# Optimization experiments

Measured on AMD Instinct MI355X. Metric: run time of the kernel, lower is better.

Reference implementation:

```python
import jax, jax.numpy as jnp
import numpy as np

TOPK = 13
ALPHA = 1.0
BETA = 6.0
CENTER_RADIUS = 0.5
EPS = 1e-7
IMG = 2048
STRIDES = (8, 16, 32)


def _make_anchor_points():
    pts = []
    for s in STRIDES:
        n = IMG // s
        c = (jnp.arange(n, dtype=jnp.float32) + 0.5) * s
        yy, xx = jnp.meshgrid(c, c, indexing='ij')
        pts.append(jnp.stack([xx.ravel(), yy.ravel()], axis=-1))
    return jnp.concatenate(pts, axis=0)  # [86016, 2]


def setup_inputs() -> dict:
    key = jax.random.key(0)
    k = jax.random.split(key, 6)
    anchor_points = _make_anchor_points()           # [P, 2]
    P = anchor_points.shape[0]
    C, G = 365, 100
    pred_scores = jax.random.normal(k[0], (P, C), dtype=jnp.float32) * 2.0 - 2.0
    pred_objectness = jax.random.normal(k[1], (P,), dtype=jnp.float32)
    # predicted boxes: anchor +- positive ltrb distances (valid xyxy)
    dist = jax.random.uniform(k[2], (P, 4), minval=2.0, maxval=120.0, dtype=jnp.float32)
    pred_boxes = jnp.concatenate([anchor_points - dist[:, :2], anchor_points + dist[:, 2:]], axis=-1)
    ctr = jax.random.uniform(k[3], (G, 2), minval=64.0, maxval=IMG - 64.0, dtype=jnp.float32)
    half = jax.random.uniform(k[4], (G, 2), minval=16.0, maxval=160.0, dtype=jnp.float32)
    gt_boxes = jnp.concatenate([ctr - half, ctr + half], axis=-1)  # [G, 4] xyxy
    gt_labels = jax.random.randint(k[5], (G,), 0, C, dtype=jnp.int64)
    valid_class_mask = jnp.ones((C,), dtype=bool)
    return {
        'pred_scores': pred_scores,
        'pred_boxes': pred_boxes,
        'pred_objectness': pred_objectness,
        'anchor_points': anchor_points,
        'gt_boxes': gt_boxes,
        'gt_labels': gt_labels,
        'valid_class_mask': valid_class_mask,
    }


def _iou_matrix(gt_boxes, pred_boxes):
    # gt: [G,4], pred: [P,4] -> [G,P]
    lt = jnp.maximum(gt_boxes[:, None, :2], pred_boxes[None, :, :2])
    rb = jnp.minimum(gt_boxes[:, None, 2:], pred_boxes[None, :, 2:])
    wh = jnp.clip(rb - lt, 0.0)
    inter = wh[..., 0] * wh[..., 1]
    area_g = jnp.prod(jnp.clip(gt_boxes[:, 2:] - gt_boxes[:, :2], 0.0), axis=-1)
    area_p = jnp.prod(jnp.clip(pred_boxes[:, 2:] - pred_boxes[:, :2], 0.0), axis=-1)
    union = area_g[:, None] + area_p[None, :] - inter
    return inter / (union + EPS)


def reference(pred_scores, pred_boxes, pred_objectness, anchor_points, gt_boxes, gt_labels, valid_class_mask):
    P, C = pred_scores.shape
    G = gt_boxes.shape[0]
    gt_labels = gt_labels.astype(jnp.int32)

    valid_gt = (gt_labels >= 0) & (gt_labels < C) & valid_class_mask[jnp.clip(gt_labels, 0, C - 1)]

    # inside-box mask [G, P]
    ax, ay = anchor_points[:, 0], anchor_points[:, 1]
    inside = ((ax[None, :] >= gt_boxes[:, 0:1]) & (ax[None, :] <= gt_boxes[:, 2:3]) &
              (ay[None, :] >= gt_boxes[:, 1:2]) & (ay[None, :] <= gt_boxes[:, 3:4]))

    gt_center = (gt_boxes[:, :2] + gt_boxes[:, 2:]) * 0.5               # [G,2]
    half_size = jnp.clip((gt_boxes[:, 2:] - gt_boxes[:, :2]) * 0.5, 1.0)
    center_delta = jnp.abs(anchor_points[None, :, :] - gt_center[:, None, :]) / half_size[:, None, :]  # [G,P,2]
    cd_max = center_delta.max(axis=-1)                                   # [G,P]
    center_mask = cd_max <= CENTER_RADIUS

    strict = inside & center_mask
    has_center = strict.any(axis=1, keepdims=True)                       # [G,1]
    cand = jnp.where(has_center, strict, inside)                         # fallback to inside-only

    iou = _iou_matrix(gt_boxes, pred_boxes)                              # [G,P]
    cls_scores = jax.nn.sigmoid(pred_scores[:, jnp.clip(gt_labels, 0, C - 1)].T)  # [G,P]
    pred_obj = jax.nn.sigmoid(pred_objectness)                           # [P]
    quality = jnp.sqrt(jnp.clip(pred_obj[None, :] * cls_scores, 0.0))
    center_prior = jnp.exp(-0.5 * jnp.sum(center_delta ** 2, axis=-1))   # [G,P]
    align = (quality ** ALPHA) * (iou ** BETA) * center_prior            # [G,P], >= 0

    masked = jnp.where(cand & valid_gt[:, None], align, -1.0)
    top_val, top_idx = jax.lax.top_k(masked, TOPK)                       # [G,TOPK]
    # scatter per-GT top-k back to [G,P]; entries with value -1 (non-candidates) stay excluded
    sel = jnp.full((G, P), -1.0, dtype=align.dtype)
    sel = sel.at[jnp.arange(G)[:, None], top_idx].set(jnp.where(top_val > -0.5, top_val, -1.0))

    # sequential 'override only if strictly greater' == per-point argmax with ties to earliest GT
    metric = sel.max(axis=0)                                             # [P]
    best_gt = jnp.argmax(sel, axis=0)                                    # [P]
    fg_mask = metric > -0.5

    overlap = iou[best_gt, jnp.arange(P)]                                # [P]
    matched_gt_indices = jnp.where(fg_mask, best_gt, -1)
    matched_labels = jnp.where(fg_mask, gt_labels[best_gt], -1)

    target_boxes = jnp.where(fg_mask[:, None], gt_boxes[best_gt], 0.0)   # [P,4]
    lab_idx = jnp.clip(matched_labels, 0, C - 1)
    score_val = jnp.where(fg_mask, jnp.clip(overlap, 0.1), 0.0)
    target_scores = jnp.zeros((P, C), dtype=pred_scores.dtype).at[jnp.arange(P), lab_idx].set(score_val)

    return (target_scores, target_boxes, fg_mask, matched_gt_indices, matched_labels)
```

## Files before the change

### kernel.cpp

```cpp
#include <hip/hip_runtime.h>
#include <cstdint>
#include <cstddef>

#define TOPK 13
#define MAXC 2816
#define NLEV 3
#define NZB  1948

__global__ __launch_bounds__(256) void pdl_zero_topk_kernel(
    const float*  __restrict__ scores,
    const float4* __restrict__ pboxes,
    const float*  __restrict__ obj,
    const float4* __restrict__ gtb,
    const int*    __restrict__ glab,
    const unsigned char* __restrict__ vmask,
    unsigned long long* __restrict__ ws_keys,
    float* __restrict__ out,
    int C, int G, long long nfloat4)
{
    const int bid = blockIdx.x;
    const int tid = threadIdx.x;

    if (bid >= G) {
        float4* dst = (float4*)out;
        const float4 z = make_float4(0.0f, 0.0f, 0.0f, 0.0f);
        const long long chunk = (nfloat4 + NZB - 1) / NZB;
        long long s0 = (long long)(bid - G) * chunk;
        long long s1 = s0 + chunk; if (s1 > nfloat4) s1 = nfloat4;
        for (long long i = s0 + tid; i < s1; i += 1024) {
            dst[i] = z;
            if (i + 256 < s1) dst[i + 256] = z;
            if (i + 512 < s1) dst[i + 512] = z;
            if (i + 768 < s1) dst[i + 768] = z;
        }
        return;
    }

    const int g = bid;
    if (tid < TOPK) ws_keys[g * TOPK + tid] = 0ULL;

    const float4 gb = gtb[g];
    const int lab = glab[g];
    bool valid = (lab >= 0) && (lab < C);
    if (valid) {
        valid = (vmask[lab] != 0) || (vmask[4 * (size_t)lab] != 0) ||
                (vmask[8 * (size_t)lab] != 0);
    }
    if (!valid) return;

    __shared__ int s_flag;
    __shared__ int s_count;
    __shared__ unsigned long long s_merge[4 * TOPK];
    __shared__ unsigned long long s_keys[MAXC];

    if (tid == 0) { s_flag = 0; s_count = 0; }

    const float cx = (gb.x + gb.z) * 0.5f;
    const float cy = (gb.y + gb.w) * 0.5f;
    const float hx = fmaxf((gb.z - gb.x) * 0.5f, 1.0f);
    const float hy = fmaxf((gb.w - gb.y) * 0.5f, 1.0f);
    const float area_g = fmaxf(gb.z - gb.x, 0.0f) * fmaxf(gb.w - gb.y, 0.0f);

    const int ls[NLEV]   = {8, 16, 32};
    const int ln[NLEV]   = {256, 128, 64};
    const int loff[NLEV] = {0, 65536, 81920};
    int x0[NLEV], y0[NLEV], ww[NLEV], cnt[NLEV];
    int T = 0;
    #pragma unroll
    for (int l = 0; l < NLEV; ++l) {
        const float fs = (float)ls[l];
        int xa = (int)floorf(gb.x / fs - 0.5f);
        int xb = (int)ceilf (gb.z / fs - 0.5f);
        int ya = (int)floorf(gb.y / fs - 0.5f);
        int yb = (int)ceilf (gb.w / fs - 0.5f);
        xa = xa > 0 ? xa : 0;
        ya = ya > 0 ? ya : 0;
        xb = xb < ln[l] - 1 ? xb : ln[l] - 1;
        yb = yb < ln[l] - 1 ? yb : ln[l] - 1;
        int w = xb - xa + 1; if (w < 0) w = 0;
        int h = yb - ya + 1; if (h < 0) h = 0;
        x0[l] = xa; y0[l] = ya; ww[l] = w;
        cnt[l] = w * h;
        T += cnt[l];
    }
    __syncthreads();

    bool any_strict = false;
    for (int j = tid; j < T; j += 256) {
        int jj = j, l = 0;
        if (jj >= cnt[0]) { jj -= cnt[0]; l = 1; if (jj >= cnt[1]) { jj -= cnt[1]; l = 2; } }
        const int iy = jj / ww[l];
        const int ix = jj - iy * ww[l];
        const float fs = (float)ls[l];
        const float ax = ((float)(x0[l] + ix) + 0.5f) * fs;
        const float ay = ((float)(y0[l] + iy) + 0.5f) * fs;
        if (ax >= gb.x && ax <= gb.z && ay >= gb.y && ay <= gb.w) {
            const float cdx = fabsf(ax - cx) / hx;
            const float cdy = fabsf(ay - cy) / hy;
            if (fmaxf(cdx, cdy) <= 0.5f) any_strict = true;
        }
    }
    if (any_strict) s_flag = 1;
    __syncthreads();
    const bool has_center = (s_flag != 0);

    for (int j = tid; j < T; j += 256) {
        int jj = j, l = 0;
        if (jj >= cnt[0]) { jj -= cnt[0]; l = 1; if (jj >= cnt[1]) { jj -= cnt[1]; l = 2; } }
        const int iy = jj / ww[l];
        const int ix = jj - iy * ww[l];
        const float fs = (float)ls[l];
        const float ax = ((float)(x0[l] + ix) + 0.5f) * fs;
        const float ay = ((float)(y0[l] + iy) + 0.5f) * fs;
        if (!(ax >= gb.x && ax <= gb.z && ay >= gb.y && ay <= gb.w)) continue;
        const float cdx = fabsf(ax - cx) / hx;
        const float cdy = fabsf(ay - cy) / hy;
        const bool strict = fmaxf(cdx, cdy) <= 0.5f;
        if (has_center && !strict) continue;

        const int p = loff[l] + (y0[l] + iy) * ln[l] + (x0[l] + ix);
        const float4 pb = pboxes[p];
        const float so = 1.0f / (1.0f + expf(-obj[p]));
        const float sc = 1.0f / (1.0f + expf(-scores[(size_t)p * C + lab]));
        const float prior = expf(-0.5f * (cdx * cdx + cdy * cdy));
        const float ltx = fmaxf(gb.x, pb.x);
        const float lty = fmaxf(gb.y, pb.y);
        const float rbx = fminf(gb.z, pb.z);
        const float rby = fminf(gb.w, pb.w);
        const float wi = fmaxf(rbx - ltx, 0.0f);
        const float hi = fmaxf(rby - lty, 0.0f);
        const float inter = wi * hi;
        const float area_p = fmaxf(pb.z - pb.x, 0.0f) * fmaxf(pb.w - pb.y, 0.0f);
        const float iou = inter / (area_g + area_p - inter + 1e-7f);
        const float q = sqrtf(fmaxf(so * sc, 0.0f));
        const float i2 = iou * iou;
        const float align = q * (i2 * i2 * i2) * prior;

        const unsigned long long key =
            ((unsigned long long)__float_as_uint(align) << 32)
          | (unsigned long long)(0xFFFFFFFFu ^ (unsigned)p);
        const int slot = atomicAdd(&s_count, 1);
        if (slot < MAXC) s_keys[slot] = key;
    }
    __syncthreads();
    const int M = s_count < MAXC ? s_count : MAXC;

    const int wid  = tid >> 6;
    const int lane = tid & 63;

    unsigned long long best = 0ULL; int bi = -1;
    for (int i = tid; i < M; i += 256) {
        const unsigned long long k = s_keys[i];
        if (k > best) { best = k; bi = i; }
    }
    for (int r = 0; r < TOPK; ++r) {
        unsigned long long wb = best;
        #pragma unroll
        for (int d = 32; d >= 1; d >>= 1) {
            const unsigned long long o = __shfl_xor(wb, d, 64);
            if (o > wb) wb = o;
        }
        if (lane == 0) s_merge[wid * TOPK + r] = wb;
        if (wb != 0ULL && best == wb) {
            s_keys[bi] = 0ULL;
            best = 0ULL; bi = -1;
            for (int i = tid; i < M; i += 256) {
                const unsigned long long k = s_keys[i];
                if (k > best) { best = k; bi = i; }
            }
        }
    }
    __syncthreads();

    if (wid == 0) {
        unsigned long long v = (lane < 4 * TOPK) ? s_merge[lane] : 0ULL;
        for (int r = 0; r < TOPK; ++r) {
            unsigned long long wb = v;
            #pragma unroll
            for (int d = 32; d >= 1; d >>= 1) {
                const unsigned long long o = __shfl_xor(wb, d, 64);
                if (o > wb) wb = o;
            }
            if (lane == 0) ws_keys[g * TOPK + r] = wb;
            if (v == wb) v = 0ULL;
        }
    }
}

__global__ __launch_bounds__(256) void pdl_finalize_kernel(
    const float4* __restrict__ pboxes,
    const float4* __restrict__ gtb,
    const int*    __restrict__ glab,
    const unsigned long long* __restrict__ ws_keys,
    float* __restrict__ out,
    int P, int C, int G)
{
    const int tid = threadIdx.x;
    const int p0  = blockIdx.x * 256;
    const int p   = p0 + tid;

    __shared__ unsigned long long s_best[256];
    s_best[tid] = 0ULL;
    __syncthreads();

    const int npairs = G * TOPK;
    for (int j = tid; j < npairs; j += 256) {
        const unsigned long long k = ws_keys[j];
        if (k == 0ULL) continue;
        const unsigned pp = 0xFFFFFFFFu ^ (unsigned)(k & 0xFFFFFFFFull);
        const int d = (int)pp - p0;
        if (d >= 0 && d < 256) {
            const int g = j / TOPK;
            const unsigned long long key2 =
                (k & 0xFFFFFFFF00000000ull) |
                (unsigned long long)(0xFFFFFFFFu - (unsigned)g);
            atomicMax(&s_best[d], key2);
        }
    }
    __syncthreads();

    if (p < P) {
        const unsigned long long k = s_best[tid];
        const bool fg = (k != 0ULL);
        float4 tb = make_float4(0.0f, 0.0f, 0.0f, 0.0f);
        float mgi = -1.0f, mlab = -1.0f;
        if (fg) {
            const int bg = (int)(0xFFFFFFFFu - (unsigned)(k & 0xFFFFFFFFull));
            const float4 gbx = gtb[bg];
            const float4 pb  = pboxes[p];
            const float ltx = fmaxf(gbx.x, pb.x);
            const float lty = fmaxf(gbx.y, pb.y);
            const float rbx = fminf(gbx.z, pb.z);
            const float rby = fminf(gbx.w, pb.w);
            const float wi = fmaxf(rbx - ltx, 0.0f);
            const float hi = fmaxf(rby - lty, 0.0f);
            const float inter = wi * hi;
            const float ag = fmaxf(gbx.z - gbx.x, 0.0f) * fmaxf(gbx.w - gbx.y, 0.0f);
            const float ap = fmaxf(pb.z - pb.x, 0.0f) * fmaxf(pb.w - pb.y, 0.0f);
            const float iou = inter / (ag + ap - inter + 1e-7f);
            const int lb = glab[bg];
            tb   = gbx;
            mgi  = (float)bg;
            mlab = (float)lb;
            int lbc = lb < 0 ? 0 : (lb > C - 1 ? C - 1 : lb);
            out[(size_t)p * C + lbc] = fmaxf(iou, 0.1f);
        }
        float4* boxes_out = (float4*)(out + (size_t)P * C);
        boxes_out[p] = tb;
        const size_t base = (size_t)P * C + (size_t)4 * P;
        out[base + p]                 = fg ? 1.0f : 0.0f;
        out[base + (size_t)P + p]     = mgi;
        out[base + (size_t)2 * P + p] = mlab;
    }
}

extern "C" void kernel_launch(void* const* d_in, const int* in_sizes, int n_in,
                              void* d_out, int out_size, void* d_ws, size_t ws_size,
                              hipStream_t stream)
{
    (void)n_in; (void)out_size; (void)ws_size;

    const float*  scores = (const float*)d_in[0];
    const float4* pboxes = (const float4*)d_in[1];
    const float*  obj    = (const float*)d_in[2];
    const float4* gtb    = (const float4*)d_in[4];
    const int*    glab   = (const int*)d_in[5];
    const unsigned char* vmask = (const unsigned char*)d_in[6];

    const int P = in_sizes[2];
    const int C = in_sizes[0] / P;
    const int G = in_sizes[5];

    unsigned long long* ws_keys = (unsigned long long*)d_ws;
    float* out = (float*)d_out;

    const long long nfloat4 = ((long long)P * C) / 4;

    pdl_zero_topk_kernel<<<G + NZB, 256, 0, stream>>>(scores, pboxes, obj, gtb,
                                                      glab, vmask, ws_keys, out,
                                                      C, G, nfloat4);
    pdl_finalize_kernel<<<(P + 255) / 256, 256, 0, stream>>>(pboxes, gtb, glab,
                                                             ws_keys, out, P, C, G);
}
```

Measured before the change: 38.98 us.

## Move score-tensor zeroing into finalize kernel, fusing zero-fill with one-hot writes

The large target_scores zero-fill moves out of the top-k kernel and into the second kernel. Each score block zeroes its own contiguous slice and then writes the one-hot IoU values for the rows it covers, after resolving per-point winners in shared memory. Separate blocks handle the per-point box, mask and index outputs in chunks of 1344 points. The top-k kernel now launches only G blocks. Before, the zero-fill ran concurrently with top-k. Now it is serialized after top-k, and every score block scans all G*TOPK keys, so the overlap is lost in exchange for fusing the scatter writes with the zero-fill.

```diff
diff --git a/kernel.cpp b/kernel.cpp
--- a/kernel.cpp
+++ b/kernel.cpp
@@ -5,9 +5,11 @@
 #define TOPK 13
 #define MAXC 2816
 #define NLEV 3
-#define NZB  1948
-
-__global__ __launch_bounds__(256) void pdl_zero_topk_kernel(
+#define SCB  2016
+#define APB  1344
+#define NROWMAX 64
+
+__global__ __launch_bounds__(256) void pdl_topk_kernel(
     const float*  __restrict__ scores,
     const float4* __restrict__ pboxes,
     const float*  __restrict__ obj,
@@ -15,28 +17,11 @@
     const int*    __restrict__ glab,
     const unsigned char* __restrict__ vmask,
     unsigned long long* __restrict__ ws_keys,
-    float* __restrict__ out,
-    int C, int G, long long nfloat4)
+    int C)
 {
-    const int bid = blockIdx.x;
+    const int g   = blockIdx.x;
     const int tid = threadIdx.x;
 
-    if (bid >= G) {
-        float4* dst = (float4*)out;
-        const float4 z = make_float4(0.0f, 0.0f, 0.0f, 0.0f);
-        const long long chunk = (nfloat4 + NZB - 1) / NZB;
-        long long s0 = (long long)(bid - G) * chunk;
-        long long s1 = s0 + chunk; if (s1 > nfloat4) s1 = nfloat4;
-        for (long long i = s0 + tid; i < s1; i += 1024) {
-            dst[i] = z;
-            if (i + 256 < s1) dst[i + 256] = z;
-            if (i + 512 < s1) dst[i + 512] = z;
-            if (i + 768 < s1) dst[i + 768] = z;
-        }
-        return;
-    }
-
-    const int g = bid;
     if (tid < TOPK) ws_keys[g * TOPK + tid] = 0ULL;
 
     const float4 gb = gtb[g];
@@ -187,7 +172,7 @@
     }
 }
 
-__global__ __launch_bounds__(256) void pdl_finalize_kernel(
+__global__ __launch_bounds__(256) void pdl_write_kernel(
     const float4* __restrict__ pboxes,
     const float4* __restrict__ gtb,
     const int*    __restrict__ glab,
@@ -195,37 +180,50 @@
     float* __restrict__ out,
     int P, int C, int G)
 {
+    const int bid = blockIdx.x;
     const int tid = threadIdx.x;
-    const int p0  = blockIdx.x * 256;
-    const int p   = p0 + tid;
-
-    __shared__ unsigned long long s_best[256];
-    s_best[tid] = 0ULL;
-    __syncthreads();
-
     const int npairs = G * TOPK;
-    for (int j = tid; j < npairs; j += 256) {
-        const unsigned long long k = ws_keys[j];
-        if (k == 0ULL) continue;
-        const unsigned pp = 0xFFFFFFFFu ^ (unsigned)(k & 0xFFFFFFFFull);
-        const int d = (int)pp - p0;
-        if (d >= 0 && d < 256) {
-            const int g = j / TOPK;
-            const unsigned long long key2 =
-                (k & 0xFFFFFFFF00000000ull) |
-                (unsigned long long)(0xFFFFFFFFu - (unsigned)g);
-            atomicMax(&s_best[d], key2);
-        }
-    }
-    __syncthreads();
-
-    if (p < P) {
-        const unsigned long long k = s_best[tid];
-        const bool fg = (k != 0ULL);
-        float4 tb = make_float4(0.0f, 0.0f, 0.0f, 0.0f);
-        float mgi = -1.0f, mlab = -1.0f;
-        if (fg) {
+
+    __shared__ unsigned long long s_best[APB];
+
+    if (bid < SCB) {
+        const long long nf4 = ((long long)P * C) >> 2;
+        const long long chunk = (nf4 + SCB - 1) / SCB;
+        const long long s0 = (long long)bid * chunk;
+        long long s1 = s0 + chunk; if (s1 > nf4) s1 = nf4;
+        if (s0 >= s1) return;
+
+        const int r0 = (int)((s0 * 4) / C);
+        const int r1 = (int)((s1 * 4 - 1) / C);
+        const int nrows = r1 - r0 + 1;
+
+        __shared__ int   s_hcol[NROWMAX];
+        __shared__ float s_hval[NROWMAX];
+        unsigned long long* s_row = s_best;
+
+        for (int i = tid; i < nrows; i += 256) s_row[i] = 0ULL;
+        __syncthreads();
+
+        for (int j = tid; j < npairs; j += 256) {
+            const unsigned long long k = ws_keys[j];
+            if (k == 0ULL) continue;
+            const unsigned pp = 0xFFFFFFFFu ^ (unsigned)(k & 0xFFFFFFFFull);
+            const int d = (int)pp - r0;
+            if (d >= 0 && d < nrows) {
+                const int g = j / TOPK;
+                const unsigned long long key2 =
+                    (k & 0xFFFFFFFF00000000ull) |
+                    (unsigned long long)(0xFFFFFFFFu - (unsigned)g);
+                atomicMax(&s_row[d], key2);
+            }
+        }
+        __syncthreads();
+
+        for (int i = tid; i < nrows; i += 256) {
+            const unsigned long long k = s_row[i];
+            if (k == 0ULL) continue;
             const int bg = (int)(0xFFFFFFFFu - (unsigned)(k & 0xFFFFFFFFull));
+            const int p  = r0 + i;
             const float4 gbx = gtb[bg];
             const float4 pb  = pboxes[p];
             const float ltx = fmaxf(gbx.x, pb.x);
@@ -238,16 +236,70 @@
             const float ag = fmaxf(gbx.z - gbx.x, 0.0f) * fmaxf(gbx.w - gbx.y, 0.0f);
             const float ap = fmaxf(pb.z - pb.x, 0.0f) * fmaxf(pb.w - pb.y, 0.0f);
             const float iou = inter / (ag + ap - inter + 1e-7f);
-            const int lb = glab[bg];
-            tb   = gbx;
+            int lb = glab[bg];
+            lb = lb < 0 ? 0 : (lb > C - 1 ? C - 1 : lb);
+            s_hcol[i] = lb;
+            s_hval[i] = fmaxf(iou, 0.1f);
+        }
+
+        float4* dst = (float4*)out;
+        const float4 z = make_float4(0.0f, 0.0f, 0.0f, 0.0f);
+        for (long long i = s0 + tid; i < s1; i += 1024) {
+            dst[i] = z;
+            if (i + 256 < s1) dst[i + 256] = z;
+            if (i + 512 < s1) dst[i + 512] = z;
+            if (i + 768 < s1) dst[i + 768] = z;
+        }
+        __syncthreads();
+
+        for (int i = tid; i < nrows; i += 256) {
+            if (s_row[i] != 0ULL) {
+                const long long f = (long long)(r0 + i) * C + s_hcol[i];
+                if (f >= s0 * 4 && f < s1 * 4)
+                    out[f] = s_hval[i];
+            }
+        }
+        return;
+    }
+
+    const int a0 = (bid - SCB) * APB;
+    int a1 = a0 + APB; if (a1 > P) a1 = P;
+    const int na = a1 - a0;
+    if (na <= 0) return;
+
+    for (int i = tid; i < na; i += 256) s_best[i] = 0ULL;
+    __syncthreads();
+
+    for (int j = tid; j < npairs; j += 256) {
+        const unsigned long long k = ws_keys[j];
+        if (k == 0ULL) continue;
+        const unsigned pp = 0xFFFFFFFFu ^ (unsigned)(k & 0xFFFFFFFFull);
+        const int d = (int)pp - a0;
+        if (d >= 0 && d < na) {
+            const int g = j / TOPK;
+            const unsigned long long key2 =
+                (k & 0xFFFFFFFF00000000ull) |
+                (unsigned long long)(0xFFFFFFFFu - (unsigned)g);
+            atomicMax(&s_best[d], key2);
+        }
+    }
+    __syncthreads();
+
+    float4* boxes_out = (float4*)(out + (size_t)P * C);
+    const size_t base = (size_t)P * C + (size_t)4 * P;
+    for (int i = tid; i < na; i += 256) {
+        const int p = a0 + i;
+        const unsigned long long k = s_best[i];
+        const bool fg = (k != 0ULL);
+        float4 tb = make_float4(0.0f, 0.0f, 0.0f, 0.0f);
+        float mgi = -1.0f, mlab = -1.0f;
+        if (fg) {
+            const int bg = (int)(0xFFFFFFFFu - (unsigned)(k & 0xFFFFFFFFull));
+            tb   = gtb[bg];
             mgi  = (float)bg;
-            mlab = (float)lb;
-            int lbc = lb < 0 ? 0 : (lb > C - 1 ? C - 1 : lb);
-            out[(size_t)p * C + lbc] = fmaxf(iou, 0.1f);
-        }
-        float4* boxes_out = (float4*)(out + (size_t)P * C);
+            mlab = (float)glab[bg];
+        }
         boxes_out[p] = tb;
-        const size_t base = (size_t)P * C + (size_t)4 * P;
         out[base + p]                 = fg ? 1.0f : 0.0f;
         out[base + (size_t)P + p]     = mgi;
         out[base + (size_t)2 * P + p] = mlab;
@@ -274,11 +326,10 @@
     unsigned long long* ws_keys = (unsigned long long*)d_ws;
     float* out = (float*)d_out;
 
-    const long long nfloat4 = ((long long)P * C) / 4;
-
-    pdl_zero_topk_kernel<<<G + NZB, 256, 0, stream>>>(scores, pboxes, obj, gtb,
-                                                      glab, vmask, ws_keys, out,
-                                                      C, G, nfloat4);
-    pdl_finalize_kernel<<<(P + 255) / 256, 256, 0, stream>>>(pboxes, gtb, glab,
-                                                             ws_keys, out, P, C, G);
+    const int ACB = (P + APB - 1) / APB;
+
+    pdl_topk_kernel<<<G, 256, 0, stream>>>(scores, pboxes, obj, gtb, glab,
+                                           vmask, ws_keys, C);
+    pdl_write_kernel<<<SCB + ACB, 256, 0, stream>>>(pboxes, gtb, glab, ws_keys,
+                                                    out, P, C, G);
 }
```

After: 45.64 us. 1.17x slower.

## Fuse center-check and candidate scoring into one pass with wave-aggregated atomics

Applied to the files above, without the earlier changes.

Merges the two passes over in-box anchors into one: each candidate is scored immediately and tagged with a strict-center bit in the top bit of its sort key, so strict candidates rank above non-strict ones. The strict-only filtering is applied at the end when writing the top-k results. Shared-memory slot allocation now uses one atomic per wavefront via ballot and popcount instead of one per thread. The cost is that non-strict candidates are always scored, and more keys may fill the MAXC buffer.

```diff
diff --git a/kernel.cpp b/kernel.cpp
--- a/kernel.cpp
+++ b/kernel.cpp
@@ -6,6 +6,7 @@
 #define MAXC 2816
 #define NLEV 3
 #define NZB  1948
+#define STRICT_BIT 0x8000000000000000ull
 
 __global__ __launch_bounds__(256) void pdl_zero_topk_kernel(
     const float*  __restrict__ scores,
@@ -85,6 +86,9 @@
     }
     __syncthreads();
 
+    const int lane = tid & 63;
+    const int wid  = tid >> 6;
+
     bool any_strict = false;
     for (int j = tid; j < T; j += 256) {
         int jj = j, l = 0;
@@ -94,59 +98,53 @@
         const float fs = (float)ls[l];
         const float ax = ((float)(x0[l] + ix) + 0.5f) * fs;
         const float ay = ((float)(y0[l] + iy) + 0.5f) * fs;
-        if (ax >= gb.x && ax <= gb.z && ay >= gb.y && ay <= gb.w) {
+        const bool inside = (ax >= gb.x && ax <= gb.z && ay >= gb.y && ay <= gb.w);
+
+        unsigned long long key = 0ULL;
+        if (inside) {
             const float cdx = fabsf(ax - cx) / hx;
             const float cdy = fabsf(ay - cy) / hy;
-            if (fmaxf(cdx, cdy) <= 0.5f) any_strict = true;
+            const bool strict = fmaxf(cdx, cdy) <= 0.5f;
+            any_strict |= strict;
+
+            const int p = loff[l] + (y0[l] + iy) * ln[l] + (x0[l] + ix);
+            const float4 pb = pboxes[p];
+            const float so = 1.0f / (1.0f + expf(-obj[p]));
+            const float sc = 1.0f / (1.0f + expf(-scores[(size_t)p * C + lab]));
+            const float prior = expf(-0.5f * (cdx * cdx + cdy * cdy));
+            const float ltx = fmaxf(gb.x, pb.x);
+            const float lty = fmaxf(gb.y, pb.y);
+            const float rbx = fminf(gb.z, pb.z);
+            const float rby = fminf(gb.w, pb.w);
+            const float wi = fmaxf(rbx - ltx, 0.0f);
+            const float hi = fmaxf(rby - lty, 0.0f);
+            const float inter = wi * hi;
+            const float area_p = fmaxf(pb.z - pb.x, 0.0f) * fmaxf(pb.w - pb.y, 0.0f);
+            const float iou = inter / (area_g + area_p - inter + 1e-7f);
+            const float q = sqrtf(fmaxf(so * sc, 0.0f));
+            const float i2 = iou * iou;
+            const float align = q * (i2 * i2 * i2) * prior;
+
+            key = (strict ? STRICT_BIT : 0ULL)
+                | ((unsigned long long)__float_as_uint(align) << 32)
+                | (unsigned long long)(0xFFFFFFFFu ^ (unsigned)p);
+        }
+
+        const unsigned long long m = __ballot(inside);
+        if (m) {
+            int base;
+            if (lane == 0) base = atomicAdd(&s_count, __popcll(m));
+            base = __shfl(base, 0, 64);
+            if (inside) {
+                const int slot = base + __popcll(m & ((1ULL << lane) - 1));
+                if (slot < MAXC) s_keys[slot] = key;
+            }
         }
     }
     if (any_strict) s_flag = 1;
     __syncthreads();
     const bool has_center = (s_flag != 0);
-
-    for (int j = tid; j < T; j += 256) {
-        int jj = j, l = 0;
-        if (jj >= cnt[0]) { jj -= cnt[0]; l = 1; if (jj >= cnt[1]) { jj -= cnt[1]; l = 2; } }
-        const int iy = jj / ww[l];
-        const int ix = jj - iy * ww[l];
-        const float fs = (float)ls[l];
-        const float ax = ((float)(x0[l] + ix) + 0.5f) * fs;
-        const float ay = ((float)(y0[l] + iy) + 0.5f) * fs;
-        if (!(ax >= gb.x && ax <= gb.z && ay >= gb.y && ay <= gb.w)) continue;
-        const float cdx = fabsf(ax - cx) / hx;
-        const float cdy = fabsf(ay - cy) / hy;
-        const bool strict = fmaxf(cdx, cdy) <= 0.5f;
-        if (has_center && !strict) continue;
-
-        const int p = loff[l] + (y0[l] + iy) * ln[l] + (x0[l] + ix);
-        const float4 pb = pboxes[p];
-        const float so = 1.0f / (1.0f + expf(-obj[p]));
-        const float sc = 1.0f / (1.0f + expf(-scores[(size_t)p * C + lab]));
-        const float prior = expf(-0.5f * (cdx * cdx + cdy * cdy));
-        const float ltx = fmaxf(gb.x, pb.x);
-        const float lty = fmaxf(gb.y, pb.y);
-        const float rbx = fminf(gb.z, pb.z);
-        const float rby = fminf(gb.w, pb.w);
-        const float wi = fmaxf(rbx - ltx, 0.0f);
-        const float hi = fmaxf(rby - lty, 0.0f);
-        const float inter = wi * hi;
-        const float area_p = fmaxf(pb.z - pb.x, 0.0f) * fmaxf(pb.w - pb.y, 0.0f);
-        const float iou = inter / (area_g + area_p - inter + 1e-7f);
-        const float q = sqrtf(fmaxf(so * sc, 0.0f));
-        const float i2 = iou * iou;
-        const float align = q * (i2 * i2 * i2) * prior;
-
-        const unsigned long long key =
-            ((unsigned long long)__float_as_uint(align) << 32)
-          | (unsigned long long)(0xFFFFFFFFu ^ (unsigned)p);
-        const int slot = atomicAdd(&s_count, 1);
-        if (slot < MAXC) s_keys[slot] = key;
-    }
-    __syncthreads();
     const int M = s_count < MAXC ? s_count : MAXC;
-
-    const int wid  = tid >> 6;
-    const int lane = tid & 63;
 
     unsigned long long best = 0ULL; int bi = -1;
     for (int i = tid; i < M; i += 256) {
@@ -181,7 +179,12 @@
                 const unsigned long long o = __shfl_xor(wb, d, 64);
                 if (o > wb) wb = o;
             }
-            if (lane == 0) ws_keys[g * TOPK + r] = wb;
+            if (lane == 0) {
+                unsigned long long w = wb;
+                if (has_center)
+                    w = (w & STRICT_BIT) ? (w & ~STRICT_BIT) : 0ULL;
+                ws_keys[g * TOPK + r] = w;
+            }
             if (v == wb) v = 0ULL;
         }
     }
```

Measured after the change: 45.22 us. 16.0% more time.

## Keep candidate keys in registers and use threshold-based top-k; flatten zero fill

Applied to the files above, without the earlier changes.

Per-GT candidate keys are now held in a fixed register array of ten per thread instead of being appended to shared memory with an atomic counter. Top-k selection repeatedly takes the largest key below the previous winner, removing the rescans of shared memory. The zero-fill blocks now each write a fixed 1024 float4 chunk, which launches many more blocks. Candidates beyond 2560 per GT are silently dropped, and the higher register use may lower occupancy.

```diff
diff --git a/kernel.cpp b/kernel.cpp
--- a/kernel.cpp
+++ b/kernel.cpp
@@ -3,9 +3,10 @@
 #include <cstddef>
 
 #define TOPK 13
-#define MAXC 2816
+#define MAXC 2560
+#define NITER 10
 #define NLEV 3
-#define NZB  1948
+#define FILL_F4 1024
 
 __global__ __launch_bounds__(256) void pdl_zero_topk_kernel(
     const float*  __restrict__ scores,
@@ -24,15 +25,12 @@
     if (bid >= G) {
         float4* dst = (float4*)out;
         const float4 z = make_float4(0.0f, 0.0f, 0.0f, 0.0f);
-        const long long chunk = (nfloat4 + NZB - 1) / NZB;
-        long long s0 = (long long)(bid - G) * chunk;
-        long long s1 = s0 + chunk; if (s1 > nfloat4) s1 = nfloat4;
-        for (long long i = s0 + tid; i < s1; i += 1024) {
-            dst[i] = z;
-            if (i + 256 < s1) dst[i + 256] = z;
-            if (i + 512 < s1) dst[i + 512] = z;
-            if (i + 768 < s1) dst[i + 768] = z;
-        }
+        const long long s0 = (long long)(bid - G) * FILL_F4;
+        const long long i = s0 + tid;
+        if (i       < nfloat4) dst[i]       = z;
+        if (i + 256 < nfloat4) dst[i + 256] = z;
+        if (i + 512 < nfloat4) dst[i + 512] = z;
+        if (i + 768 < nfloat4) dst[i + 768] = z;
         return;
     }
 
@@ -49,11 +47,9 @@
     if (!valid) return;
 
     __shared__ int s_flag;
-    __shared__ int s_count;
     __shared__ unsigned long long s_merge[4 * TOPK];
-    __shared__ unsigned long long s_keys[MAXC];
-
-    if (tid == 0) { s_flag = 0; s_count = 0; }
+
+    if (tid == 0) s_flag = 0;
 
     const float cx = (gb.x + gb.z) * 0.5f;
     const float cy = (gb.y + gb.w) * 0.5f;
@@ -85,6 +81,9 @@
     }
     __syncthreads();
 
+    const int lane = tid & 63;
+    const int wid  = tid >> 6;
+
     bool any_strict = false;
     for (int j = tid; j < T; j += 256) {
         int jj = j, l = 0;
@@ -104,7 +103,12 @@
     __syncthreads();
     const bool has_center = (s_flag != 0);
 
-    for (int j = tid; j < T; j += 256) {
+    unsigned long long k[NITER];
+    #pragma unroll
+    for (int it = 0; it < NITER; ++it) {
+        k[it] = 0ULL;
+        const int j = tid + (it << 8);
+        if (j >= T) continue;
         int jj = j, l = 0;
         if (jj >= cnt[0]) { jj -= cnt[0]; l = 1; if (jj >= cnt[1]) { jj -= cnt[1]; l = 2; } }
         const int iy = jj / ww[l];
@@ -136,53 +140,42 @@
         const float i2 = iou * iou;
         const float align = q * (i2 * i2 * i2) * prior;
 
-        const unsigned long long key =
-            ((unsigned long long)__float_as_uint(align) << 32)
-          | (unsigned long long)(0xFFFFFFFFu ^ (unsigned)p);
-        const int slot = atomicAdd(&s_count, 1);
-        if (slot < MAXC) s_keys[slot] = key;
-    }
-    __syncthreads();
-    const int M = s_count < MAXC ? s_count : MAXC;
-
-    const int wid  = tid >> 6;
-    const int lane = tid & 63;
-
-    unsigned long long best = 0ULL; int bi = -1;
-    for (int i = tid; i < M; i += 256) {
-        const unsigned long long k = s_keys[i];
-        if (k > best) { best = k; bi = i; }
-    }
-    for (int r = 0; r < TOPK; ++r) {
-        unsigned long long wb = best;
-        #pragma unroll
-        for (int d = 32; d >= 1; d >>= 1) {
-            const unsigned long long o = __shfl_xor(wb, d, 64);
-            if (o > wb) wb = o;
-        }
-        if (lane == 0) s_merge[wid * TOPK + r] = wb;
-        if (wb != 0ULL && best == wb) {
-            s_keys[bi] = 0ULL;
-            best = 0ULL; bi = -1;
-            for (int i = tid; i < M; i += 256) {
-                const unsigned long long k = s_keys[i];
-                if (k > best) { best = k; bi = i; }
+        k[it] = ((unsigned long long)__float_as_uint(align) << 32)
+              | (unsigned long long)(0xFFFFFFFFu ^ (unsigned)p);
+    }
+
+    {
+        unsigned long long W = ~0ULL;
+        for (int r = 0; r < TOPK; ++r) {
+            unsigned long long loc = 0ULL;
+            #pragma unroll
+            for (int it = 0; it < NITER; ++it)
+                if (k[it] < W && k[it] > loc) loc = k[it];
+            unsigned long long wb = loc;
+            #pragma unroll
+            for (int d = 32; d >= 1; d >>= 1) {
+                const unsigned long long o = __shfl_xor(wb, d, 64);
+                if (o > wb) wb = o;
             }
+            if (lane == 0) s_merge[wid * TOPK + r] = wb;
+            W = wb;
         }
     }
     __syncthreads();
 
     if (wid == 0) {
-        unsigned long long v = (lane < 4 * TOPK) ? s_merge[lane] : 0ULL;
+        const unsigned long long v =
+            (lane < 4 * TOPK) ? s_merge[lane] : 0ULL;
+        unsigned long long W = ~0ULL;
         for (int r = 0; r < TOPK; ++r) {
-            unsigned long long wb = v;
+            unsigned long long wb = (v < W) ? v : 0ULL;
             #pragma unroll
             for (int d = 32; d >= 1; d >>= 1) {
                 const unsigned long long o = __shfl_xor(wb, d, 64);
                 if (o > wb) wb = o;
             }
             if (lane == 0) ws_keys[g * TOPK + r] = wb;
-            if (v == wb) v = 0ULL;
+            W = wb;
         }
     }
 }
@@ -275,6 +268,7 @@
     float* out = (float*)d_out;
 
     const long long nfloat4 = ((long long)P * C) / 4;
+    const int NZB = (int)((nfloat4 + FILL_F4 - 1) / FILL_F4);
 
     pdl_zero_topk_kernel<<<G + NZB, 256, 0, stream>>>(scores, pboxes, obj, gtb,
                                                       glab, vmask, ws_keys, out,
```

After: 36.46 us, median of 2. 6.5% less time.
